# Performance work log

Measured on AMD Instinct MI355X. Metric: run time of the kernel, lower is better.

## Reference

```python
import jax, jax.numpy as jnp
import numpy as np

EPS_BN = 1e-5
EPS_ENT = 1e-15


def _gcn(x, src, dst, ew, W, b):
    # GCNConv: add self-loops (weight 1), symmetric deg^-1/2 normalization, aggregate x@W.
    n = x.shape[0]
    h = x @ W
    loop = jnp.arange(n)
    s2 = jnp.concatenate([src, loop])
    d2 = jnp.concatenate([dst, loop])
    we2 = jnp.concatenate([ew, jnp.ones((n,), x.dtype)])
    deg = jax.ops.segment_sum(we2, d2, num_segments=n)
    dinv = jnp.where(deg > 0, jax.lax.rsqrt(jnp.maximum(deg, 1e-12)), 0.0)
    coef = dinv[s2] * we2 * dinv[d2]
    return jax.ops.segment_sum(h[s2] * coef[:, None], d2, num_segments=n) + b


def _bn(x, g, be):
    # BatchNorm over the node dimension (training-mode batch stats)
    m = jnp.mean(x, axis=0)
    v = jnp.var(x, axis=0)
    return (x - m) * jax.lax.rsqrt(v + EPS_BN) * g + be


def _block(x, src, dst, ew, W, b, g, be):
    return jax.nn.silu(_bn(_gcn(x, src, dst, ew, W, b), g, be))


def _stoch_pool(x, src, dst, ew, Wp, bp, gp, bep):
    # DiffPool-style: soft cluster assignments from a ResidualBlock, pooled features/adjacency,
    # link loss ||A - S S^T||_F / N^2 (computed sparsely) and mean assignment entropy.
    n = x.shape[0]
    s = jax.nn.softmax(_block(x, src, dst, ew, Wp, bp, gp, bep), axis=-1)  # [n, K]
    K = s.shape[1]
    xp = s.T @ x  # [K, C]
    sw = s[src] * ew[:, None]  # [E, K]
    a_pool = sw.T @ s[dst]  # [K, K] = S^T A S
    cross = jnp.trace(a_pool)  # <A, S S^T>
    sts = s.T @ s  # [K, K]; ||S S^T||_F^2 = ||S^T S||_F^2
    link = jnp.sqrt(jnp.maximum(jnp.sum(ew * ew) - 2.0 * cross + jnp.sum(sts * sts), 0.0)) / (n * n)
    ent = jnp.mean(jnp.sum(-s * jnp.log(s + EPS_ENT), axis=-1))
    grid = jnp.arange(K)
    src_n = jnp.repeat(grid, K)
    dst_n = jnp.tile(grid, K)
    return xp, src_n, dst_n, a_pool.reshape(-1), link, ent


def _level(x, src, dst, ew, Wa, ba, ga, bea, Wb, bb, gb, beb, Wp, bp, gp, bep):
    x = _block(x, src, dst, ew, Wa, ba, ga, bea)
    x = x + _block(x, src, dst, ew, Wb, bb, gb, beb)  # pool_after-1 = 1 residual block
    return _stoch_pool(x, src, dst, ew, Wp, bp, gp, bep)


def setup_inputs() -> dict:
    key = jax.random.key(0)
    ks = jax.random.split(key, 10)
    N, E, IN, CH, K1, K2, OUT = 20000, 640000, 128, 128, 256, 64, 10
    lin = lambda k, fi, fo: (jax.random.normal(k, (fi, fo), jnp.float32) / np.sqrt(fi)).astype(jnp.float32)
    z = lambda c: jnp.zeros((c,), jnp.float32)
    o = lambda c: jnp.ones((c,), jnp.float32)
    d = {
        'x': jax.random.normal(ks[0], (N, IN), jnp.float32),
        'edge_index': jax.random.randint(ks[1], (2, E), 0, N, jnp.int32),
        'batch': jnp.zeros((N,), jnp.int32),
        'batch_ptr': jnp.array([0, N], jnp.int32),
        'W1a': lin(ks[2], IN, CH), 'b1a': z(CH), 'g1a': o(CH), 'be1a': z(CH),
        'W1b': lin(ks[3], CH, CH), 'b1b': z(CH), 'g1b': o(CH), 'be1b': z(CH),
        'Wp1': lin(ks[4], CH, K1), 'bp1': z(K1), 'gp1': o(K1), 'bep1': z(K1),
        'W2a': lin(ks[5], CH, CH), 'b2a': z(CH), 'g2a': o(CH), 'be2a': z(CH),
        'W2b': lin(ks[6], CH, CH), 'b2b': z(CH), 'g2b': o(CH), 'be2b': z(CH),
        'Wp2': lin(ks[7], CH, K2), 'bp2': z(K2), 'gp2': o(K2), 'bep2': z(K2),
        'Wlin': lin(ks[8], CH, OUT), 'blin': z(OUT),
    }
    return d


def reference(x, edge_index, batch, batch_ptr,
              W1a, b1a, g1a, be1a, W1b, b1b, g1b, be1b, Wp1, bp1, gp1, bep1,
              W2a, b2a, g2a, be2a, W2b, b2b, g2b, be2b, Wp2, bp2, gp2, bep2,
              Wlin, blin):
    src, dst = edge_index[0], edge_index[1]
    ew = jnp.ones(src.shape, x.dtype)  # level-1 edge_weight is None -> ones
    x, src, dst, ew, l1, e1 = _level(x, src, dst, ew, W1a, b1a, g1a, be1a,
                                     W1b, b1b, g1b, be1b, Wp1, bp1, gp1, bep1)
    x, src, dst, ew, l2, e2 = _level(x, src, dst, ew, W2a, b2a, g2a, be2a,
                                     W2b, b2b, g2b, be2b, Wp2, bp2, gp2, bep2)
    pooled = jnp.mean(x, axis=0, keepdims=True)  # global_mean_pool, single graph (B=1)
    logits = pooled @ Wlin + blin
    return jax.nn.log_softmax(logits, axis=1), (e1 + e2) + (l1 + l2)
```

## Files before the change

kernel.cpp:

```cpp
#include <hip/hip_runtime.h>

#define EPS_BN 1e-5f
typedef unsigned int uint;
typedef unsigned short ushort;
typedef __attribute__((ext_vector_type(8))) short bf16x8;
typedef __attribute__((ext_vector_type(4))) float f32x4;

__device__ inline ushort f2bf(float f) {
  uint u = __float_as_uint(f);
  uint r = (u + 0x7FFFu + ((u >> 16) & 1u)) >> 16;
  return (ushort)r;
}
__device__ inline float bflo(uint h) { return __uint_as_float(h << 16); }
__device__ inline float bfhi(uint h) { return __uint_as_float(h & 0xFFFF0000u); }


__global__ void k_hist(const int* __restrict__ idx, int* __restrict__ cnt, int E) {
  int e = blockIdx.x * blockDim.x + threadIdx.x;
  if (e < E) atomicAdd(&cnt[idx[e]], 1);
}

__global__ __launch_bounds__(1024) void k_scan(
    const int* __restrict__ cnt, int* __restrict__ rowptr, int* __restrict__ cursor,
    int N, int E) {
  __shared__ int sh[1024];
  int t = threadIdx.x;
  int chunk = (N + 1023) / 1024;
  int i0 = t * chunk, i1 = min(i0 + chunk, N);
  int s = 0;
  for (int i = i0; i < i1; ++i) s += cnt[i];
  sh[t] = s; __syncthreads();
  for (int o = 1; o < 1024; o <<= 1) {
    int v = (t >= o) ? sh[t - o] : 0;
    __syncthreads();
    sh[t] += v;
    __syncthreads();
  }
  int run = (t == 0) ? 0 : sh[t - 1];
  for (int i = i0; i < i1; ++i) { rowptr[i] = run; cursor[i] = run; run += cnt[i]; }
  if (t == 1023) rowptr[N] = E;
}

__global__ void k_fill_csr(const int* __restrict__ key, const int* __restrict__ val,
                           int* __restrict__ cursor, int* __restrict__ col, int E) {
  int e = blockIdx.x * blockDim.x + threadIdx.x;
  if (e < E) {
    int pos = atomicAdd(&cursor[key[e]], 1);
    col[pos] = val[e];
  }
}

__global__ void k_dinv_cnt(const int* __restrict__ cnt, float* __restrict__ dinv, int n) {
  int i = blockIdx.x * blockDim.x + threadIdx.x;
  if (i < n) dinv[i] = rsqrtf(1.0f + (float)cnt[i]);
}


__global__ void k_gather_agg_b2(const int* __restrict__ rowptr, const int* __restrict__ col,
                                const float* __restrict__ dinv, const ushort* __restrict__ H,
                                float* __restrict__ out, int C2) {
  int d = blockIdx.x;
  int c2 = threadIdx.x;
  const uint* H2 = (const uint*)H;
  int b = rowptr[d], e = rowptr[d + 1];
  float a0 = 0.f, a1 = 0.f;
#pragma unroll 4
  for (int i = b; i < e; ++i) {
    int s = col[i];
    float dv = dinv[s];
    uint h = H2[(size_t)s * C2 + c2];
    a0 += dv * bflo(h);
    a1 += dv * bfhi(h);
  }
  float dd = dinv[d];
  uint hd = H2[(size_t)d * C2 + c2];
  float2 o;
  o.x = dd * a0 + dd * dd * bflo(hd);
  o.y = dd * a1 + dd * dd * bfhi(hd);
  *(float2*)(out + (size_t)d * (C2 * 2) + c2 * 2) = o;
}

__global__ void k_gather_agg_b2b(const int* __restrict__ rowptr, const int* __restrict__ col,
                                 const float* __restrict__ dinv, const ushort* __restrict__ H,
                                 ushort* __restrict__ out, int C2) {
  int d = blockIdx.x;
  int c2 = threadIdx.x;
  const uint* H2 = (const uint*)H;
  int b = rowptr[d], e = rowptr[d + 1];
  float a0 = 0.f, a1 = 0.f;
#pragma unroll 4
  for (int i = b; i < e; ++i) {
    int s = col[i];
    float dv = dinv[s];
    uint h = H2[(size_t)s * C2 + c2];
    a0 += dv * bflo(h);
    a1 += dv * bfhi(h);
  }
  float dd = dinv[d];
  uint hd = H2[(size_t)d * C2 + c2];
  ushort2 o;
  o.x = f2bf(dd * a0 + dd * dd * bflo(hd));
  o.y = f2bf(dd * a1 + dd * dd * bfhi(hd));
  *(ushort2*)(out + (size_t)d * (C2 * 2) + c2 * 2) = o;
}

__global__ void k_gather_T_b2(const int* __restrict__ rowptr, const int* __restrict__ col,
                              const ushort* __restrict__ S, float* __restrict__ T, int C2) {
  int s = blockIdx.x;
  int c2 = threadIdx.x;
  const uint* S2 = (const uint*)S;
  int b = rowptr[s], e = rowptr[s + 1];
  float a0 = 0.f, a1 = 0.f;
#pragma unroll 4
  for (int i = b; i < e; ++i) {
    int d = col[i];
    uint h = S2[(size_t)d * C2 + c2];
    a0 += bflo(h);
    a1 += bfhi(h);
  }
  float2 o; o.x = a0; o.y = a1;
  *(float2*)(T + (size_t)s * (C2 * 2) + c2 * 2) = o;
}


__global__ void k_conv(const float* __restrict__ in, ushort* __restrict__ out, int n4) {
  int i = blockIdx.x * blockDim.x + threadIdx.x;
  if (i < n4) {
    float4 v = ((const float4*)in)[i];
    ushort4 o;
    o.x = f2bf(v.x); o.y = f2bf(v.y); o.z = f2bf(v.z); o.w = f2bf(v.w);
    ((ushort4*)out)[i] = o;
  }
}

__global__ void k_tconv(const float* __restrict__ in, ushort* __restrict__ out,
                        int R, int Cc) {
  __shared__ float tile[32][33];
  int c0 = blockIdx.x * 32, r0 = blockIdx.y * 32;
  int tx = threadIdx.x, ty = threadIdx.y;
  for (int i = 0; i < 32; i += 8) {
    int r = r0 + ty + i, c = c0 + tx;
    if (r < R && c < Cc) tile[ty + i][tx] = in[(size_t)r * Cc + c];
  }
  __syncthreads();
  for (int i = 0; i < 32; i += 8) {
    int oc = c0 + ty + i;
    int orr = r0 + tx;
    if (oc < Cc && orr < R) out[(size_t)oc * R + orr] = f2bf(tile[tx][ty + i]);
  }
}

__global__ __launch_bounds__(256) void k_mfma_nt(
    const ushort* __restrict__ A, const ushort* __restrict__ B, float* __restrict__ C,
    ushort* __restrict__ Cb, int I, int J, int K, int kChunk, int atom) {
  __shared__ ushort As[64][40];
  __shared__ ushort Bs[64][40];
  int t = threadIdx.x;
  int w = t >> 6, l = t & 63;
  int i0 = blockIdx.y * 64, j0 = blockIdx.x * 64;
  int k0 = blockIdx.z * kChunk;
  int k1 = min(k0 + kChunk, K);
  f32x4 acc[4] = {};
  int lrow = t >> 2;
  int lk = (t & 3) * 8;
  for (int kk = k0; kk < k1; kk += 32) {
    uint4 av = make_uint4(0u, 0u, 0u, 0u);
    int ar = i0 + lrow;
    if (ar < I) av = *(const uint4*)(A + (size_t)ar * K + kk + lk);
    uint4 bv = *(const uint4*)(B + (size_t)(j0 + lrow) * K + kk + lk);
    *(uint4*)&As[lrow][lk] = av;
    *(uint4*)&Bs[lrow][lk] = bv;
    __syncthreads();
    bf16x8 af = *(const bf16x8*)&As[16 * w + (l & 15)][(l >> 4) * 8];
#pragma unroll
    for (int jt = 0; jt < 4; ++jt) {
      bf16x8 bf = *(const bf16x8*)&Bs[16 * jt + (l & 15)][(l >> 4) * 8];
      acc[jt] = __builtin_amdgcn_mfma_f32_16x16x32_bf16(af, bf, acc[jt], 0, 0, 0);
    }
    __syncthreads();
  }
  int rbase = i0 + 16 * w + ((l >> 4) * 4);
  int cbase = j0 + (l & 15);
#pragma unroll
  for (int jt = 0; jt < 4; ++jt) {
#pragma unroll
    for (int rr = 0; rr < 4; ++rr) {
      int r = rbase + rr;
      if (r < I) {
        size_t idx = (size_t)r * J + jt * 16 + cbase;
        if (Cb) Cb[idx] = f2bf(acc[jt][rr]);
        else if (atom) atomicAdd(&C[idx], acc[jt][rr]);
        else C[idx] = acc[jt][rr];
      }
    }
  }
}

__global__ __launch_bounds__(256) void k_sgemm_nn(
    const float* __restrict__ A, const float* __restrict__ B, float* __restrict__ C,
    int M, int N, int K) {
  __shared__ float As[16][64];
  __shared__ float Bs[16][68];
  int t = threadIdx.x;
  int tx = t & 15, ty = t >> 4;
  int row0 = blockIdx.y * 64, col0 = blockIdx.x * 64;
  float acc[4][4] = {};
  for (int k0 = 0; k0 < K; k0 += 16) {
    int ar = t >> 2;
    int ak = (t & 3) * 4;
    float4 av = make_float4(0.f, 0.f, 0.f, 0.f);
    if (row0 + ar < M) av = *(const float4*)(A + (size_t)(row0 + ar) * K + k0 + ak);
    As[ak + 0][ar] = av.x; As[ak + 1][ar] = av.y;
    As[ak + 2][ar] = av.z; As[ak + 3][ar] = av.w;
    int bk = t >> 4;
    int bc = (t & 15) * 4;
    float4 bv = *(const float4*)(B + (size_t)(k0 + bk) * N + col0 + bc);
    *(float4*)&Bs[bk][bc] = bv;
    __syncthreads();
#pragma unroll
    for (int k = 0; k < 16; ++k) {
      float a[4], b[4];
#pragma unroll
      for (int u = 0; u < 4; ++u) a[u] = As[k][ty * 4 + u];
#pragma unroll
      for (int v = 0; v < 4; ++v) b[v] = Bs[k][tx * 4 + v];
#pragma unroll
      for (int u = 0; u < 4; ++u)
#pragma unroll
        for (int v = 0; v < 4; ++v) acc[u][v] += a[u] * b[v];
    }
    __syncthreads();
  }
#pragma unroll
  for (int u = 0; u < 4; ++u) {
    int r = row0 + ty * 4 + u;
    if (r < M) {
#pragma unroll
      for (int v = 0; v < 4; ++v) C[(size_t)r * N + col0 + tx * 4 + v] = acc[u][v];
    }
  }
}


__global__ void k_col_stats2(const float* __restrict__ X, const float* __restrict__ bias,
                             float* __restrict__ part, int M, int C, int rpb) {
  int c = threadIdx.x;
  int b = blockIdx.x;
  int r0 = b * rpb, r1 = min(r0 + rpb, M);
  float bi = bias[c];
  float s = 0.f, sq = 0.f;
  for (int r = r0; r < r1; ++r) {
    float v = X[(size_t)r * C + c] + bi;
    s += v; sq += v * v;
  }
  part[(size_t)b * 2 * C + c] = s;
  part[(size_t)b * 2 * C + C + c] = sq;
}

__global__ __launch_bounds__(256) void k_colred_par(
    const float* __restrict__ part, int nblk, int C,
    float* __restrict__ cs, float* __restrict__ csq) {
  __shared__ float sh[256];
  int c = blockIdx.x;
  int t = threadIdx.x;
  float s = 0.f, sq = 0.f;
  for (int b = t; b < nblk; b += 256) {
    s  += part[(size_t)b * 2 * C + c];
    sq += part[(size_t)b * 2 * C + C + c];
  }
  sh[t] = s; __syncthreads();
  for (int o = 128; o > 0; o >>= 1) { if (t < o) sh[t] += sh[t + o]; __syncthreads(); }
  if (t == 0) cs[c] = sh[0];
  __syncthreads();
  sh[t] = sq; __syncthreads();
  for (int o = 128; o > 0; o >>= 1) { if (t < o) sh[t] += sh[t + o]; __syncthreads(); }
  if (t == 0) csq[c] = sh[0];
}

__global__ void k_bn_silu(const float* __restrict__ X, const float* __restrict__ bias,
                          const float* __restrict__ cs, const float* __restrict__ csq,
                          const float* __restrict__ g, const float* __restrict__ be,
                          const float* __restrict__ resid, float* __restrict__ out,
                          ushort* __restrict__ outb,
                          int tot, int cmask, float invM) {
  int i = blockIdx.x * blockDim.x + threadIdx.x;
  if (i >= tot) return;
  int c = i & cmask;
  float m = cs[c] * invM;
  float var = csq[c] * invM - m * m;
  float v = (X[i] + bias[c] - m) * rsqrtf(var + EPS_BN) * g[c] + be[c];
  float y = v / (1.f + expf(-v));
  if (resid) y += resid[i];
  out[i] = y;
  if (outb) outb[i] = f2bf(y);
}

__global__ __launch_bounds__(256) void k_bn_small(
    const float* __restrict__ X, const float* __restrict__ bias,
    const float* __restrict__ g, const float* __restrict__ be,
    const float* __restrict__ resid, float* __restrict__ out,
    int M, int C, float invM) {
  __shared__ float sh[256];
  int c = blockIdx.x;
  int t = threadIdx.x;
  bool act = t < M;
  float v = 0.f;
  if (act) v = X[(size_t)t * C + c] + bias[c];
  sh[t] = v; __syncthreads();
  for (int o = 128; o > 0; o >>= 1) { if (t < o) sh[t] += sh[t + o]; __syncthreads(); }
  float m = sh[0] * invM; __syncthreads();
  sh[t] = v * v; __syncthreads();
  for (int o = 128; o > 0; o >>= 1) { if (t < o) sh[t] += sh[t + o]; __syncthreads(); }
  float var = sh[0] * invM - m * m;
  if (act) {
    float y = (v - m) * rsqrtf(var + EPS_BN) * g[c] + be[c];
    y = y / (1.f + expf(-y));
    if (resid) y += resid[(size_t)t * C + c];
    out[(size_t)t * C + c] = y;
  }
}

template <int C>
__global__ void k_softmax_ent3(float* __restrict__ X, ushort* __restrict__ outb,
                               float* __restrict__ part, int nrows) {
  constexpr int VPT = C / 64;
  __shared__ float went[4];
  int gt = blockIdx.x * blockDim.x + threadIdx.x;
  int row = gt >> 6;
  int l = gt & 63;
  int wid = threadIdx.x >> 6;
  bool active = row < nrows;
  size_t base = active ? (size_t)row * C : 0;
  float d[VPT];
  if (VPT == 4) {
    float4 v = *(const float4*)(X + base + l * 4);
    d[0] = v.x; d[1] = v.y; d[2] = v.z; d[3] = v.w;
  } else {
    d[0] = X[base + l];
  }
  float mx = d[0];
#pragma unroll
  for (int i = 1; i < VPT; ++i) mx = fmaxf(mx, d[i]);
  for (int o = 32; o > 0; o >>= 1) mx = fmaxf(mx, __shfl_xor(mx, o));
  float se = 0.f;
  float e[VPT];
#pragma unroll
  for (int i = 0; i < VPT; ++i) { d[i] -= mx; e[i] = expf(d[i]); se += e[i]; }
  for (int o = 32; o > 0; o >>= 1) se += __shfl_xor(se, o);
  float inv = 1.f / se;
  float pd = 0.f;
#pragma unroll
  for (int i = 0; i < VPT; ++i) { e[i] *= inv; pd += e[i] * d[i]; }
  if (active) {
    if (VPT == 4) {
      float4 v; v.x = e[0]; v.y = e[1]; v.z = e[2]; v.w = e[3];
      *(float4*)(X + base + l * 4) = v;
      if (outb) {
        ushort4 u; u.x = f2bf(e[0]); u.y = f2bf(e[1]); u.z = f2bf(e[2]); u.w = f2bf(e[3]);
        *(ushort4*)(outb + base + l * 4) = u;
      }
    } else {
      X[base + l] = e[0];
      if (outb) outb[base + l] = f2bf(e[0]);
    }
  }
  for (int o = 32; o > 0; o >>= 1) pd += __shfl_xor(pd, o);
  if (l == 0) went[wid] = active ? (logf(se) - pd) : 0.f;
  __syncthreads();
  if (threadIdx.x == 0) part[blockIdx.x] = went[0] + went[1] + went[2] + went[3];
}

__global__ __launch_bounds__(256) void k_reduce_atom(
    const float* __restrict__ in, int n, float* __restrict__ out) {
  __shared__ float sh[256];
  int t = threadIdx.x;
  int per = (n + gridDim.x - 1) / gridDim.x;
  int i0 = blockIdx.x * per, i1 = min(i0 + per, n);
  float s = 0.f;
  for (int i = i0 + t; i < i1; i += 256) s += in[i];
  sh[t] = s; __syncthreads();
  for (int o = 128; o > 0; o >>= 1) { if (t < o) sh[t] += sh[t + o]; __syncthreads(); }
  if (t == 0) atomicAdd(out, sh[0]);
}

__global__ __launch_bounds__(256) void k_scalN_par(
    const float* __restrict__ P0, const float* __restrict__ P1, int K,
    float* __restrict__ outb, int Z) {
  __shared__ float sh[256];
  int b = blockIdx.x, t = threadIdx.x;
  float s = 0.f;
  int slot;
  if (b == 0) {
    slot = 0;
    for (int i = t; i < K; i += 256) s += P0[(size_t)i * K + i];
  } else {
    int which = (b - 1) / Z;
    int chunk = (b - 1) % Z;
    slot = 1 + which;
    const float4* P4 = (const float4*)(which ? P0 : P1);
    int n4 = (K * K) >> 2;
    int per = (n4 + Z - 1) / Z;
    int i0 = chunk * per, i1 = min(i0 + per, n4);
    for (int i = i0 + t; i < i1; i += 256) {
      float4 v = P4[i];
      s += v.x * v.x + v.y * v.y + v.z * v.z + v.w * v.w;
    }
  }
  sh[t] = s; __syncthreads();
  for (int o = 128; o > 0; o >>= 1) { if (t < o) sh[t] += sh[t + o]; __syncthreads(); }
  if (t == 0) atomicAdd(&outb[slot], sh[0]);
}

__global__ __launch_bounds__(256) void k_scal2_par(
    const float* __restrict__ U, const float* __restrict__ V, int n,
    const float* __restrict__ P, int nP, float* __restrict__ outb, int Z) {
  __shared__ float sh[256];
  int b = blockIdx.x, t = threadIdx.x;
  float s = 0.f;
  int slot;
  if (b < Z) {
    slot = 0;
    const float4* U4 = (const float4*)U;
    const float4* V4 = (const float4*)V;
    int n4 = n >> 2;
    int per = (n4 + Z - 1) / Z;
    int i0 = b * per, i1 = min(i0 + per, n4);
    for (int i = i0 + t; i < i1; i += 256) {
      float4 u = U4[i], v = V4[i];
      s += u.x * v.x + u.y * v.y + u.z * v.z + u.w * v.w;
    }
  } else {
    slot = 1;
    const float4* P4 = (const float4*)P;
    int n4 = nP >> 2;
    for (int i = t; i < n4; i += 256) {
      float4 v = P4[i];
      s += v.x * v.x + v.y * v.y + v.z * v.z + v.w * v.w;
    }
  }
  sh[t] = s; __syncthreads();
  for (int o = 128; o > 0; o >>= 1) { if (t < o) sh[t] += sh[t + o]; __syncthreads(); }
  if (t == 0) atomicAdd(&outb[slot], sh[0]);
}


__global__ __launch_bounds__(256) void k_deg2_par(
    const float* __restrict__ A2T, float* __restrict__ dinv2, int Np) {
  __shared__ float sh[256];
  int q = blockIdx.x;
  int t = threadIdx.x;
  float s = (t == 0) ? 1.0f : 0.f;
  for (int p = t; p < Np; p += 256) s += A2T[(size_t)q * Np + p];
  sh[t] = s; __syncthreads();
  for (int o = 128; o > 0; o >>= 1) { if (t < o) sh[t] += sh[t + o]; __syncthreads(); }
  if (t == 0) {
    float d = sh[0];
    dinv2[q] = d > 0.f ? rsqrtf(fmaxf(d, 1e-12f)) : 0.f;
  }
}

__global__ void k_dense_agg(const float* __restrict__ A2T, const float* __restrict__ dinv2,
                            const float* __restrict__ H, float* __restrict__ out,
                            int Np, int C) {
  int q = blockIdx.x, c = threadIdx.x;
  float acc = 0.f;
#pragma unroll 8
  for (int p = 0; p < Np; ++p)
    acc += dinv2[p] * A2T[(size_t)q * Np + p] * H[(size_t)p * C + c];
  float dq = dinv2[q];
  out[(size_t)q * C + c] = dq * acc + dq * dq * H[(size_t)q * C + c];
}

__global__ __launch_bounds__(256) void k_tn3(
    const float* __restrict__ S, const float* __restrict__ B2,
    float* __restrict__ sts2, float* __restrict__ xp2, int M) {
  __shared__ float As[64][65];
  __shared__ float Bs[64][65];
  int z = blockIdx.x;
  const float* B; float* C; int J, j0;
  if (z == 0) { B = S;  C = sts2; J = 64;  j0 = 0; }
  else        { B = B2; C = xp2;  J = 128; j0 = (z - 1) * 64; }
  int t = threadIdx.x;
  int tj = t & 63, ti = t >> 6;
  float acc[16] = {};
  for (int m0 = 0; m0 < M; m0 += 64) {
#pragma unroll
    for (int r = 0; r < 16; ++r) {
      As[ti * 16 + r][tj] = S[(size_t)(m0 + ti * 16 + r) * 64 + tj];
      Bs[ti * 16 + r][tj] = B[(size_t)(m0 + ti * 16 + r) * J + j0 + tj];
    }
    __syncthreads();
#pragma unroll 4
    for (int mm = 0; mm < 64; ++mm) {
      float bv = Bs[mm][tj];
#pragma unroll
      for (int ii = 0; ii < 16; ++ii) acc[ii] += As[mm][ti * 16 + ii] * bv;
    }
    __syncthreads();
  }
  for (int ii = 0; ii < 16; ++ii) C[(size_t)(ti * 16 + ii) * J + j0 + tj] = acc[ii];
}

__global__ void k_final(const float* __restrict__ xp2, const float* __restrict__ Wlin,
                        const float* __restrict__ blin, const float* __restrict__ scal,
                        float* __restrict__ out, int N1, int E1, int K1, int K2, int OUT) {
  __shared__ float pooled[128];
  __shared__ float logits[32];
  int t = threadIdx.x;
  float s = 0.f;
  for (int r = 0; r < K2; ++r) s += xp2[(size_t)r * 128 + t];
  pooled[t] = s / (float)K2;
  __syncthreads();
  if (t < OUT) {
    float acc = blin[t];
    for (int k = 0; k < 128; ++k) acc += pooled[k] * Wlin[(size_t)k * OUT + t];
    logits[t] = acc;
  }
  __syncthreads();
  if (t == 0) {
    float mx = logits[0];
    for (int j = 1; j < OUT; ++j) mx = fmaxf(mx, logits[j]);
    float se = 0.f;
    for (int j = 0; j < OUT; ++j) se += expf(logits[j] - mx);
    float lse = mx + logf(se);
    for (int j = 0; j < OUT; ++j) out[j] = logits[j] - lse;
    float n1 = (float)N1;
    float ent1 = scal[0] / n1;
    float ent2 = scal[1] / (float)K1;
    float link1 = sqrtf(fmaxf((float)E1 - 2.f * scal[2] + scal[3], 0.f)) / (n1 * n1);
    float link2 = sqrtf(fmaxf(scal[4] - 2.f * scal[5] + scal[6], 0.f)) / ((float)K1 * (float)K1);
    out[OUT] = ent1 + ent2 + link1 + link2;
  }
}


extern "C" void kernel_launch(void* const* d_in, const int* in_sizes, int n_in,
                              void* d_out, int out_size, void* d_ws, size_t ws_size,
                              hipStream_t stream) {
  (void)n_in; (void)out_size; (void)ws_size;
  const float* x = (const float*)d_in[0];
  const int* ei  = (const int*)d_in[1];
  const int N = in_sizes[0] / 128;
  const int E = in_sizes[1] / 2;
  const int* src = ei;
  const int* dst = ei + E;
  const float *W1a=(const float*)d_in[4],  *b1a=(const float*)d_in[5],
              *g1a=(const float*)d_in[6],  *be1a=(const float*)d_in[7];
  const float *W1b=(const float*)d_in[8],  *b1b=(const float*)d_in[9],
              *g1b=(const float*)d_in[10], *be1b=(const float*)d_in[11];
  const float *Wp1=(const float*)d_in[12], *bp1=(const float*)d_in[13],
              *gp1=(const float*)d_in[14], *bep1=(const float*)d_in[15];
  const float *W2a=(const float*)d_in[16], *b2a=(const float*)d_in[17],
              *g2a=(const float*)d_in[18], *be2a=(const float*)d_in[19];
  const float *W2b=(const float*)d_in[20], *b2b=(const float*)d_in[21],
              *g2b=(const float*)d_in[22], *be2b=(const float*)d_in[23];
  const float *Wp2=(const float*)d_in[24], *bp2=(const float*)d_in[25],
              *gp2=(const float*)d_in[26], *bep2=(const float*)d_in[27];
  const float *Wlin=(const float*)d_in[28], *blin=(const float*)d_in[29];
  const int K1 = in_sizes[12] / 128;
  const int K2 = in_sizes[24] / 128;
  const int OUT = in_sizes[29];

  char* base = (char*)d_ws;
  size_t off = 0;
  auto allocb = [&](size_t bytes) -> void* {
    void* p = (void*)(base + off);
    off += ((bytes + 255) & ~(size_t)255);
    return p;
  };
  auto alloc = [&](size_t nf) -> float* { return (float*)allocb(nf * 4); };
  auto alloci = [&](size_t ni) -> int* { return (int*)allocb(ni * 4); };
  auto allocu = [&](size_t nu) -> ushort* { return (ushort*)allocb(nu * 2); };

  auto cdiv = [](long long a, long long b) { return (int)((a + b - 1) / b); };

  const int RPB = 16;
  const int NBLK1 = cdiv(N, RPB);

  float* scal  = alloc(16);
  float* cs    = alloc(256);
  float* csq   = alloc(256);
  float* dinv  = alloc(N);
  float* dinv2 = alloc(K1);
  float* apT   = alloc((size_t)K1 * K1);
  float* sts   = alloc((size_t)K1 * K1);
  float* xp    = alloc((size_t)K1 * 128);
  float* h2    = alloc((size_t)K1 * 128);
  float* y2    = alloc((size_t)K1 * 128);
  float* xa2   = alloc((size_t)K1 * 128);
  float* x2f   = alloc((size_t)K1 * 128);
  float* s2b   = alloc((size_t)K1 * K2);
  float* U     = alloc((size_t)K1 * K2);
  float* sts2  = alloc((size_t)K2 * K2);
  float* xp2   = alloc((size_t)K2 * 128);
  float* ent1p = alloc(cdiv(N, 4) + 8);
  float* ent2p = alloc(64 + 8);
  float* csp   = alloc((size_t)(NBLK1 + 2) * 512);
  float* R1 = alloc((size_t)N * 128);
  float* R2 = alloc((size_t)N * 128);
  float* R3 = alloc((size_t)N * K1);
  float* R4 = alloc((size_t)N * K1);
  ushort* B16A = allocu((size_t)N * 128);
  ushort* W1at = allocu(128 * 128);
  ushort* W1bt = allocu(128 * 128);
  ushort* Wp1t = allocu((size_t)K1 * 128);
  int* cnt_d = alloci(N);
  int* rp_d  = alloci(N + 1);
  int* cur_d = alloci(N);
  int* col_s = alloci(E);

  ushort* Hb   = (ushort*)R3;
  ushort* aggB = (ushort*)R3;
  ushort* Sb   = (ushort*)R3;
  ushort* St   = (ushort*)R1;
  ushort* ATSt = (ushort*)R2;
  ushort* R2t  = B16A;

  hipMemsetAsync(scal, 0, 16 * sizeof(float), stream);

  hipMemsetAsync(cnt_d, 0, (size_t)N * sizeof(int), stream);
  k_hist<<<cdiv(E, 256), 256, 0, stream>>>(dst, cnt_d, E);
  k_scan<<<1, 1024, 0, stream>>>(cnt_d, rp_d, cur_d, N, E);
  k_fill_csr<<<cdiv(E, 256), 256, 0, stream>>>(dst, src, cur_d, col_s, E);
  k_dinv_cnt<<<cdiv(N, 256), 256, 0, stream>>>(cnt_d, dinv, N);

  {
    dim3 b32(32, 8);
    k_tconv<<<dim3(4, 4), b32, 0, stream>>>(W1a, W1at, 128, 128);
    k_tconv<<<dim3(4, 4), b32, 0, stream>>>(W1b, W1bt, 128, 128);
    k_tconv<<<dim3(8, 4), b32, 0, stream>>>(Wp1, Wp1t, 128, K1);
  }
  k_conv<<<cdiv((size_t)N * 128 / 4, 256), 256, 0, stream>>>(x, B16A, N * 128 / 4);

  auto mfma_nt = [&](const ushort* A, const ushort* B, float* C, ushort* Cb,
                     int I, int J, int K, int nz) {
    int chunk = K, z = 1;
    if (nz > 1) {
      chunk = ((cdiv(K, nz) + 31) & ~31);
      z = cdiv(K, chunk);
      hipMemsetAsync(C, 0, (size_t)I * J * sizeof(float), stream);
    }
    dim3 g(J / 64, cdiv(I, 64), z);
    k_mfma_nt<<<g, 256, 0, stream>>>(A, B, C, Cb, I, J, K, chunk, z > 1 ? 1 : 0);
  };
  auto gemm_nn = [&](const float* A, const float* B, float* C, int M, int Nn, int K) {
    dim3 g(Nn / 64, cdiv(M, 64));
    k_sgemm_nn<<<g, 256, 0, stream>>>(A, B, C, M, Nn, K);
  };

  auto block1 = [&](const ushort* xin_b, const ushort* Wt, const float* b, const float* gg,
                    const float* be, const float* resid, float* outp, ushort* outb, int C) {
    mfma_nt(xin_b, Wt, nullptr, Hb, N, C, 128, 1);
    k_gather_agg_b2<<<N, C / 2, 0, stream>>>(rp_d, col_s, dinv, Hb, R4, C / 2);
    k_col_stats2<<<NBLK1, C, 0, stream>>>(R4, b, csp, N, C, RPB);
    k_colred_par<<<C, 256, 0, stream>>>(csp, NBLK1, C, cs, csq);
    int tot = N * C;
    k_bn_silu<<<cdiv(tot, 256), 256, 0, stream>>>(R4, b, cs, csq, gg, be, resid, outp,
                                                  outb, tot, C - 1, 1.f / N);
  };

  block1(B16A, W1at, b1a, g1a, be1a, nullptr, R1, B16A, 128);
  block1(B16A, W1bt, b1b, g1b, be1b, R1,      R2, B16A, 128);

  k_gather_agg_b2b<<<N, 64, 0, stream>>>(rp_d, col_s, dinv, B16A, aggB, 64);
  mfma_nt(aggB, Wp1t, R4, nullptr, N, K1, 128, 1);
  k_col_stats2<<<NBLK1, K1, 0, stream>>>(R4, bp1, csp, N, K1, RPB);
  k_colred_par<<<K1, 256, 0, stream>>>(csp, NBLK1, K1, cs, csq);
  k_bn_silu<<<cdiv(N * K1, 256), 256, 0, stream>>>(R4, bp1, cs, csq, gp1, bep1, nullptr,
                                                   R4, nullptr, N * K1, K1 - 1, 1.f / N);
  k_softmax_ent3<256><<<cdiv(N, 4), 256, 0, stream>>>(R4, Sb, ent1p, N);
  k_reduce_atom<<<8, 256, 0, stream>>>(ent1p, cdiv(N, 4), &scal[0]);

  {
    dim3 b32(32, 8);
    k_tconv<<<dim3(K1 / 32, cdiv(N, 32)), b32, 0, stream>>>(R4, St, N, K1);
    k_tconv<<<dim3(128 / 32, cdiv(N, 32)), b32, 0, stream>>>(R2, R2t, N, 128);
  }
  k_gather_T_b2<<<N, K1 / 2, 0, stream>>>(rp_d, col_s, Sb, R4, K1 / 2);
  {
    dim3 b32(32, 8);
    k_tconv<<<dim3(K1 / 32, cdiv(N, 32)), b32, 0, stream>>>(R4, ATSt, N, K1);
  }

  mfma_nt(St, ATSt, apT, nullptr, K1, K1, N, 16);
  mfma_nt(St, St,  sts,  nullptr, K1, K1, N, 16);
  mfma_nt(St, R2t, xp,   nullptr, K1, 128, N, 16);
  k_scalN_par<<<1 + 2 * 16, 256, 0, stream>>>(apT, sts, K1, &scal[2], 16);

  k_deg2_par<<<K1, 256, 0, stream>>>(apT, dinv2, K1);

  auto block2 = [&](const float* xin, const float* W, const float* b, const float* gg,
                    const float* be, const float* resid, float* outp, int C) {
    gemm_nn(xin, W, h2, K1, C, 128);
    k_dense_agg<<<K1, C, 0, stream>>>(apT, dinv2, h2, y2, K1, C);
    k_bn_small<<<C, 256, 0, stream>>>(y2, b, gg, be, resid, outp, K1, C, 1.f / K1);
  };

  block2(xp,  W2a, b2a, g2a, be2a, nullptr, xa2, 128);
  block2(xa2, W2b, b2b, g2b, be2b, xa2,     x2f, 128);
  block2(x2f, Wp2, bp2, gp2, bep2, nullptr, s2b, K2);
  k_softmax_ent3<64><<<cdiv(K1, 4), 256, 0, stream>>>(s2b, nullptr, ent2p, K1);
  k_reduce_atom<<<2, 256, 0, stream>>>(ent2p, cdiv(K1, 4), &scal[1]);

  gemm_nn(apT, s2b, U, K1, K2, K1);
  k_tn3<<<3, 256, 0, stream>>>(s2b, x2f, sts2, xp2, K1);
  k_scal2_par<<<8 + 1, 256, 0, stream>>>(U, s2b, K1 * K2, sts2, K2 * K2, &scal[5], 8);

  k_final<<<1, 128, 0, stream>>>(xp2, Wlin, blin, scal, (float*)d_out, N, E, K1, K2, OUT);
}
```

Baseline: 591.9 us.

## Fuse setup kernels, keep pooled assignments in bf16, merge three pooling GEMMs

Several small launches are merged: the histogram and the input bf16 conversion become one kernel, dinv is computed inside the scan, the three weight transposes run as one launch, and the three split-K pooling GEMMs (S^T A S, S^T S, S^T X) become a single launch with one memset. The softmax no longer writes the fp32 assignment matrix, and the transposes and the A^T S gather now read and write bf16 instead of fp32. This cuts launch overhead and memory traffic. The gather output is now rounded to bf16 before the transpose, where it used to be transposed from fp32, which slightly changes precision.

```diff
diff --git a/kernel.cpp b/kernel.cpp
--- a/kernel.cpp
+++ b/kernel.cpp
@@ -15,14 +15,26 @@
 __device__ inline float bfhi(uint h) { return __uint_as_float(h & 0xFFFF0000u); }
 
 
-__global__ void k_hist(const int* __restrict__ idx, int* __restrict__ cnt, int E) {
-  int e = blockIdx.x * blockDim.x + threadIdx.x;
-  if (e < E) atomicAdd(&cnt[idx[e]], 1);
+__global__ void k_pre(const int* __restrict__ dst, int* __restrict__ cnt, int E,
+                      const float* __restrict__ x, ushort* __restrict__ xb, int n4, int HB) {
+  int b = blockIdx.x;
+  if (b < HB) {
+    int e = b * 256 + threadIdx.x;
+    if (e < E) atomicAdd(&cnt[dst[e]], 1);
+  } else {
+    int i = (b - HB) * 256 + threadIdx.x;
+    if (i < n4) {
+      float4 v = ((const float4*)x)[i];
+      ushort4 o;
+      o.x = f2bf(v.x); o.y = f2bf(v.y); o.z = f2bf(v.z); o.w = f2bf(v.w);
+      ((ushort4*)xb)[i] = o;
+    }
+  }
 }
 
 __global__ __launch_bounds__(1024) void k_scan(
     const int* __restrict__ cnt, int* __restrict__ rowptr, int* __restrict__ cursor,
-    int N, int E) {
+    float* __restrict__ dinv, int N, int E) {
   __shared__ int sh[1024];
   int t = threadIdx.x;
   int chunk = (N + 1023) / 1024;
@@ -37,7 +49,10 @@
     __syncthreads();
   }
   int run = (t == 0) ? 0 : sh[t - 1];
-  for (int i = i0; i < i1; ++i) { rowptr[i] = run; cursor[i] = run; run += cnt[i]; }
+  for (int i = i0; i < i1; ++i) {
+    rowptr[i] = run; cursor[i] = run; run += cnt[i];
+    dinv[i] = rsqrtf(1.0f + (float)cnt[i]);
+  }
   if (t == 1023) rowptr[N] = E;
 }
 
@@ -48,11 +63,6 @@
     int pos = atomicAdd(&cursor[key[e]], 1);
     col[pos] = val[e];
   }
-}
-
-__global__ void k_dinv_cnt(const int* __restrict__ cnt, float* __restrict__ dinv, int n) {
-  int i = blockIdx.x * blockDim.x + threadIdx.x;
-  if (i < n) dinv[i] = rsqrtf(1.0f + (float)cnt[i]);
 }
 
 
@@ -104,8 +114,8 @@
   *(ushort2*)(out + (size_t)d * (C2 * 2) + c2 * 2) = o;
 }
 
-__global__ void k_gather_T_b2(const int* __restrict__ rowptr, const int* __restrict__ col,
-                              const ushort* __restrict__ S, float* __restrict__ T, int C2) {
+__global__ void k_gather_T_b2b(const int* __restrict__ rowptr, const int* __restrict__ col,
+                               const ushort* __restrict__ S, ushort* __restrict__ T, int C2) {
   int s = blockIdx.x;
   int c2 = threadIdx.x;
   const uint* S2 = (const uint*)S;
@@ -118,25 +128,57 @@
     a0 += bflo(h);
     a1 += bfhi(h);
   }
-  float2 o; o.x = a0; o.y = a1;
-  *(float2*)(T + (size_t)s * (C2 * 2) + c2 * 2) = o;
-}
-
-
-__global__ void k_conv(const float* __restrict__ in, ushort* __restrict__ out, int n4) {
-  int i = blockIdx.x * blockDim.x + threadIdx.x;
-  if (i < n4) {
-    float4 v = ((const float4*)in)[i];
-    ushort4 o;
-    o.x = f2bf(v.x); o.y = f2bf(v.y); o.z = f2bf(v.z); o.w = f2bf(v.w);
-    ((ushort4*)out)[i] = o;
-  }
-}
+  ushort2 o; o.x = f2bf(a0); o.y = f2bf(a1);
+  *(ushort2*)(T + (size_t)s * (C2 * 2) + c2 * 2) = o;
+}
+
 
 __global__ void k_tconv(const float* __restrict__ in, ushort* __restrict__ out,
                         int R, int Cc) {
   __shared__ float tile[32][33];
   int c0 = blockIdx.x * 32, r0 = blockIdx.y * 32;
+  int tx = threadIdx.x, ty = threadIdx.y;
+  for (int i = 0; i < 32; i += 8) {
+    int r = r0 + ty + i, c = c0 + tx;
+    if (r < R && c < Cc) tile[ty + i][tx] = in[(size_t)r * Cc + c];
+  }
+  __syncthreads();
+  for (int i = 0; i < 32; i += 8) {
+    int oc = c0 + ty + i;
+    int orr = r0 + tx;
+    if (oc < Cc && orr < R) out[(size_t)oc * R + orr] = f2bf(tile[tx][ty + i]);
+  }
+}
+
+__global__ void k_tconv_b(const ushort* __restrict__ in, ushort* __restrict__ out,
+                          int R, int Cc) {
+  __shared__ ushort tile[32][33];
+  int c0 = blockIdx.x * 32, r0 = blockIdx.y * 32;
+  int tx = threadIdx.x, ty = threadIdx.y;
+  for (int i = 0; i < 32; i += 8) {
+    int r = r0 + ty + i, c = c0 + tx;
+    if (r < R && c < Cc) tile[ty + i][tx] = in[(size_t)r * Cc + c];
+  }
+  __syncthreads();
+  for (int i = 0; i < 32; i += 8) {
+    int oc = c0 + ty + i;
+    int orr = r0 + tx;
+    if (oc < Cc && orr < R) out[(size_t)oc * R + orr] = tile[tx][ty + i];
+  }
+}
+
+__global__ void k_tconv3(const float* __restrict__ W0, const float* __restrict__ W1,
+                         const float* __restrict__ W2,
+                         ushort* __restrict__ O0, ushort* __restrict__ O1,
+                         ushort* __restrict__ O2, int K1) {
+  __shared__ float tile[32][33];
+  int z = blockIdx.z;
+  const float* in = (z == 0) ? W0 : (z == 1) ? W1 : W2;
+  ushort* out = (z == 0) ? O0 : (z == 1) ? O1 : O2;
+  int Cc = (z == 2) ? K1 : 128;
+  int R = 128;
+  int c0 = blockIdx.x * 32, r0 = blockIdx.y * 32;
+  if (c0 >= Cc) return;
   int tx = threadIdx.x, ty = threadIdx.y;
   for (int i = 0; i < 32; i += 8) {
     int r = r0 + ty + i, c = c0 + tx;
@@ -192,6 +234,51 @@
         else if (atom) atomicAdd(&C[idx], acc[jt][rr]);
         else C[idx] = acc[jt][rr];
       }
+    }
+  }
+}
+
+__global__ __launch_bounds__(256) void k_mfma3(
+    const ushort* __restrict__ St, const ushort* __restrict__ ATSt,
+    const ushort* __restrict__ R2t,
+    float* __restrict__ apT, float* __restrict__ sts, float* __restrict__ xp,
+    int K, int kChunk) {
+  __shared__ ushort As[64][40];
+  __shared__ ushort Bs[64][40];
+  int xb_ = blockIdx.x;
+  const ushort* B; float* C; int J, j0;
+  if (xb_ < 4)      { B = ATSt; C = apT; J = 256; j0 = xb_ * 64; }
+  else if (xb_ < 8) { B = St;   C = sts; J = 256; j0 = (xb_ - 4) * 64; }
+  else              { B = R2t;  C = xp;  J = 128; j0 = (xb_ - 8) * 64; }
+  int t = threadIdx.x;
+  int w = t >> 6, l = t & 63;
+  int i0 = blockIdx.y * 64;
+  int k0 = blockIdx.z * kChunk;
+  int k1 = min(k0 + kChunk, K);
+  f32x4 acc[4] = {};
+  int lrow = t >> 2;
+  int lk = (t & 3) * 8;
+  for (int kk = k0; kk < k1; kk += 32) {
+    uint4 av = *(const uint4*)(St + (size_t)(i0 + lrow) * K + kk + lk);
+    uint4 bv = *(const uint4*)(B + (size_t)(j0 + lrow) * K + kk + lk);
+    *(uint4*)&As[lrow][lk] = av;
+    *(uint4*)&Bs[lrow][lk] = bv;
+    __syncthreads();
+    bf16x8 af = *(const bf16x8*)&As[16 * w + (l & 15)][(l >> 4) * 8];
+#pragma unroll
+    for (int jt = 0; jt < 4; ++jt) {
+      bf16x8 bf = *(const bf16x8*)&Bs[16 * jt + (l & 15)][(l >> 4) * 8];
+      acc[jt] = __builtin_amdgcn_mfma_f32_16x16x32_bf16(af, bf, acc[jt], 0, 0, 0);
+    }
+    __syncthreads();
+  }
+  int rbase = i0 + 16 * w + ((l >> 4) * 4);
+  int cbase = j0 + (l & 15);
+#pragma unroll
+  for (int jt = 0; jt < 4; ++jt) {
+#pragma unroll
+    for (int rr = 0; rr < 4; ++rr) {
+      atomicAdd(&C[(size_t)(rbase + rr) * J + jt * 16 + cbase], acc[jt][rr]);
     }
   }
 }
@@ -322,7 +409,7 @@
 
 template <int C>
 __global__ void k_softmax_ent3(float* __restrict__ X, ushort* __restrict__ outb,
-                               float* __restrict__ part, int nrows) {
+                               float* __restrict__ part, int nrows, int writeX) {
   constexpr int VPT = C / 64;
   __shared__ float went[4];
   int gt = blockIdx.x * blockDim.x + threadIdx.x;
@@ -353,14 +440,16 @@
   for (int i = 0; i < VPT; ++i) { e[i] *= inv; pd += e[i] * d[i]; }
   if (active) {
     if (VPT == 4) {
-      float4 v; v.x = e[0]; v.y = e[1]; v.z = e[2]; v.w = e[3];
-      *(float4*)(X + base + l * 4) = v;
+      if (writeX) {
+        float4 v; v.x = e[0]; v.y = e[1]; v.z = e[2]; v.w = e[3];
+        *(float4*)(X + base + l * 4) = v;
+      }
       if (outb) {
         ushort4 u; u.x = f2bf(e[0]); u.y = f2bf(e[1]); u.z = f2bf(e[2]); u.w = f2bf(e[3]);
         *(ushort4*)(outb + base + l * 4) = u;
       }
     } else {
-      X[base + l] = e[0];
+      if (writeX) X[base + l] = e[0];
       if (outb) outb[base + l] = f2bf(e[0]);
     }
   }
@@ -612,6 +701,7 @@
   ushort* Hb   = (ushort*)R3;
   ushort* aggB = (ushort*)R3;
   ushort* Sb   = (ushort*)R3;
+  ushort* ATSb = (ushort*)R4;
   ushort* St   = (ushort*)R1;
   ushort* ATSt = (ushort*)R2;
   ushort* R2t  = B16A;
@@ -619,29 +709,23 @@
   hipMemsetAsync(scal, 0, 16 * sizeof(float), stream);
 
   hipMemsetAsync(cnt_d, 0, (size_t)N * sizeof(int), stream);
-  k_hist<<<cdiv(E, 256), 256, 0, stream>>>(dst, cnt_d, E);
-  k_scan<<<1, 1024, 0, stream>>>(cnt_d, rp_d, cur_d, N, E);
+  {
+    int HB = cdiv(E, 256);
+    int CB = cdiv((size_t)N * 128 / 4, 256);
+    k_pre<<<HB + CB, 256, 0, stream>>>(dst, cnt_d, E, x, B16A, N * 128 / 4, HB);
+  }
+  k_scan<<<1, 1024, 0, stream>>>(cnt_d, rp_d, cur_d, dinv, N, E);
   k_fill_csr<<<cdiv(E, 256), 256, 0, stream>>>(dst, src, cur_d, col_s, E);
-  k_dinv_cnt<<<cdiv(N, 256), 256, 0, stream>>>(cnt_d, dinv, N);
 
   {
     dim3 b32(32, 8);
-    k_tconv<<<dim3(4, 4), b32, 0, stream>>>(W1a, W1at, 128, 128);
-    k_tconv<<<dim3(4, 4), b32, 0, stream>>>(W1b, W1bt, 128, 128);
-    k_tconv<<<dim3(8, 4), b32, 0, stream>>>(Wp1, Wp1t, 128, K1);
-  }
-  k_conv<<<cdiv((size_t)N * 128 / 4, 256), 256, 0, stream>>>(x, B16A, N * 128 / 4);
+    k_tconv3<<<dim3(8, 4, 3), b32, 0, stream>>>(W1a, W1b, Wp1, W1at, W1bt, Wp1t, K1);
+  }
 
   auto mfma_nt = [&](const ushort* A, const ushort* B, float* C, ushort* Cb,
-                     int I, int J, int K, int nz) {
-    int chunk = K, z = 1;
-    if (nz > 1) {
-      chunk = ((cdiv(K, nz) + 31) & ~31);
-      z = cdiv(K, chunk);
-      hipMemsetAsync(C, 0, (size_t)I * J * sizeof(float), stream);
-    }
-    dim3 g(J / 64, cdiv(I, 64), z);
-    k_mfma_nt<<<g, 256, 0, stream>>>(A, B, C, Cb, I, J, K, chunk, z > 1 ? 1 : 0);
+                     int I, int J, int K) {
+    dim3 g(J / 64, cdiv(I, 64), 1);
+    k_mfma_nt<<<g, 256, 0, stream>>>(A, B, C, Cb, I, J, K, K, 0);
   };
   auto gemm_nn = [&](const float* A, const float* B, float* C, int M, int Nn, int K) {
     dim3 g(Nn / 64, cdiv(M, 64));
@@ -650,7 +734,7 @@
 
   auto block1 = [&](const ushort* xin_b, const ushort* Wt, const float* b, const float* gg,
                     const float* be, const float* resid, float* outp, ushort* outb, int C) {
-    mfma_nt(xin_b, Wt, nullptr, Hb, N, C, 128, 1);
+    mfma_nt(xin_b, Wt, nullptr, Hb, N, C, 128);
     k_gather_agg_b2<<<N, C / 2, 0, stream>>>(rp_d, col_s, dinv, Hb, R4, C / 2);
     k_col_stats2<<<NBLK1, C, 0, stream>>>(R4, b, csp, N, C, RPB);
     k_colred_par<<<C, 256, 0, stream>>>(csp, NBLK1, C, cs, csq);
@@ -663,28 +747,31 @@
   block1(B16A, W1bt, b1b, g1b, be1b, R1,      R2, B16A, 128);
 
   k_gather_agg_b2b<<<N, 64, 0, stream>>>(rp_d, col_s, dinv, B16A, aggB, 64);
-  mfma_nt(aggB, Wp1t, R4, nullptr, N, K1, 128, 1);
+  mfma_nt(aggB, Wp1t, R4, nullptr, N, K1, 128);
   k_col_stats2<<<NBLK1, K1, 0, stream>>>(R4, bp1, csp, N, K1, RPB);
   k_colred_par<<<K1, 256, 0, stream>>>(csp, NBLK1, K1, cs, csq);
   k_bn_silu<<<cdiv(N * K1, 256), 256, 0, stream>>>(R4, bp1, cs, csq, gp1, bep1, nullptr,
                                                    R4, nullptr, N * K1, K1 - 1, 1.f / N);
-  k_softmax_ent3<256><<<cdiv(N, 4), 256, 0, stream>>>(R4, Sb, ent1p, N);
+  k_softmax_ent3<256><<<cdiv(N, 4), 256, 0, stream>>>(R4, Sb, ent1p, N, 0);
   k_reduce_atom<<<8, 256, 0, stream>>>(ent1p, cdiv(N, 4), &scal[0]);
 
   {
     dim3 b32(32, 8);
-    k_tconv<<<dim3(K1 / 32, cdiv(N, 32)), b32, 0, stream>>>(R4, St, N, K1);
+    k_tconv_b<<<dim3(K1 / 32, cdiv(N, 32)), b32, 0, stream>>>(Sb, St, N, K1);
     k_tconv<<<dim3(128 / 32, cdiv(N, 32)), b32, 0, stream>>>(R2, R2t, N, 128);
   }
-  k_gather_T_b2<<<N, K1 / 2, 0, stream>>>(rp_d, col_s, Sb, R4, K1 / 2);
+  k_gather_T_b2b<<<N, K1 / 2, 0, stream>>>(rp_d, col_s, Sb, ATSb, K1 / 2);
   {
     dim3 b32(32, 8);
-    k_tconv<<<dim3(K1 / 32, cdiv(N, 32)), b32, 0, stream>>>(R4, ATSt, N, K1);
-  }
-
-  mfma_nt(St, ATSt, apT, nullptr, K1, K1, N, 16);
-  mfma_nt(St, St,  sts,  nullptr, K1, K1, N, 16);
-  mfma_nt(St, R2t, xp,   nullptr, K1, 128, N, 16);
+    k_tconv_b<<<dim3(K1 / 32, cdiv(N, 32)), b32, 0, stream>>>(ATSb, ATSt, N, K1);
+  }
+
+  {
+    hipMemsetAsync(apT, 0, (size_t)(2 * K1 * K1 + K1 * 128) * sizeof(float), stream);
+    int chunk = ((cdiv(N, 16) + 31) & ~31);
+    int z = cdiv(N, chunk);
+    k_mfma3<<<dim3(10, 4, z), 256, 0, stream>>>(St, ATSt, R2t, apT, sts, xp, N, chunk);
+  }
   k_scalN_par<<<1 + 2 * 16, 256, 0, stream>>>(apT, sts, K1, &scal[2], 16);
 
   k_deg2_par<<<K1, 256, 0, stream>>>(apT, dinv2, K1);
@@ -699,7 +786,7 @@
   block2(xp,  W2a, b2a, g2a, be2a, nullptr, xa2, 128);
   block2(xa2, W2b, b2b, g2b, be2b, xa2,     x2f, 128);
   block2(x2f, Wp2, bp2, gp2, bep2, nullptr, s2b, K2);
-  k_softmax_ent3<64><<<cdiv(K1, 4), 256, 0, stream>>>(s2b, nullptr, ent2p, K1);
+  k_softmax_ent3<64><<<cdiv(K1, 4), 256, 0, stream>>>(s2b, nullptr, ent2p, K1, 1);
   k_reduce_atom<<<2, 256, 0, stream>>>(ent2p, cdiv(K1, 4), &scal[1]);
 
   gemm_nn(apT, s2b, U, K1, K2, K1);
```

New measurement: 544.7 us. -8.0%, faster.
